# Optimization experiments

Hardware: AMD Instinct MI355X
Metric: run time of the kernel (lower is better)

Reference implementation:

```python
import jax, jax.numpy as jnp
import numpy as np

N = 150000   # total supergraph nodes (entities+events+chains)
D = 128      # embed_size
H = 4        # attention heads
DH = D // H  # head dim
E = 300000   # edges per layer
L = 4        # layer_specs length
A = 8        # edge attr dim
T = 10       # num_edge_type
TIME_SCALE = 24.0
SLOPE = 0.2  # negative_slope


def setup_inputs() -> dict:
    key = jax.random.key(0)
    ks = jax.random.split(key, 16)
    nrm = lambda k, s, sc=1.0: jax.random.normal(k, s, dtype=jnp.float32) * sc
    return {
        'x': nrm(ks[0], (N, D), 0.1),
        'Wq': nrm(ks[1], (L, D, D), D ** -0.5),
        'Wk': nrm(ks[2], (L, D, D), D ** -0.5),
        'Wv': nrm(ks[3], (L, D, D), D ** -0.5),
        'Wskip': nrm(ks[4], (L, D, D), D ** -0.5),
        'Wa': nrm(ks[5], (L, A, D), 0.1),
        'time_w': nrm(ks[6], (D,)),
        'time_b': nrm(ks[7], (D,), 0.1),
        'dist_w': nrm(ks[8], (D,)),
        'dist_b': nrm(ks[9], (D,), 0.1),
        'type_table': nrm(ks[10], (T, D), 0.1),
        'bn_gamma': jnp.ones((L, D), jnp.float32),
        'bn_beta': jnp.zeros((L, D), jnp.float32),
        'beta': jnp.full((L,), 0.5, jnp.float32),
        'edge_attr': jax.random.uniform(ks[11], (L, E, A), dtype=jnp.float32),
        'edge_dt': jax.random.uniform(ks[12], (L, E), dtype=jnp.float32) * TIME_SCALE,
        'edge_ds': jax.random.uniform(ks[13], (L, E), dtype=jnp.float32) * 10.0,
        'edge_index': jax.random.randint(ks[14], (L, 2, E), 0, N),
        'edge_type': jax.random.randint(ks[15], (L, E), 0, T),
    }


def _layer(x, Wq, Wk, Wv, Wskip, Wa, time_w, time_b, dist_w, dist_b,
           type_table, gamma, bvec, beta, attr, dt, ds, ei, et):
    n = x.shape[0]
    src, dst = ei[0], ei[1]
    # continuous time / distance encoders: cos basis (TimeEncoder / 'time' DistanceEncoder)
    te = jnp.cos((dt / TIME_SCALE)[:, None] * time_w + time_b)   # [E,D]
    de = jnp.cos(ds[:, None] * dist_w + dist_b)                  # [E,D]
    # 'add' edge/time fusion: attr MLP + time + dist + edge-type embeddings
    edge_feat = attr @ Wa + te + de + type_table[et]             # [E,D]
    kv_in = x[src] + edge_feat                                   # gather + fuse
    q = (x @ Wq).reshape(n, H, DH)[dst]                          # [E,H,DH]
    k = (kv_in @ Wk).reshape(-1, H, DH)
    v = (kv_in @ Wv).reshape(-1, H, DH)
    logits = (q * k).sum(-1) * (DH ** -0.5)                      # [E,H]
    logits = jnp.where(logits >= 0, logits, SLOPE * logits)      # leaky_relu(negative_slope)
    # segment softmax over incoming edges of each destination node
    m = jax.ops.segment_max(logits, dst, num_segments=n)
    a = jnp.exp(logits - m[dst])
    denom = jax.ops.segment_sum(a, dst, num_segments=n)
    a = a / denom[dst]
    agg = jax.ops.segment_sum(a[..., None] * v, dst, num_segments=n).reshape(n, D)
    # beta-weighted residual (learn_beta) with skip projection
    out = beta * (x @ Wskip) + (1.0 - beta) * agg
    # BatchNorm1d (training-mode batch stats) + ReLU
    mu = out.mean(0)
    var = out.var(0)
    out = (out - mu) * jax.lax.rsqrt(var + 1e-5) * gamma + bvec
    return jax.nn.relu(out)


def reference(x, Wq, Wk, Wv, Wskip, Wa, time_w, time_b, dist_w, dist_b,
              type_table, bn_gamma, bn_beta, beta, edge_attr, edge_dt,
              edge_ds, edge_index, edge_type):
    for l in range(L):  # entity2event, event2event, event2chain (time filter), chain2chain
        x = _layer(x, Wq[l], Wk[l], Wv[l], Wskip[l], Wa[l],
                   time_w, time_b, dist_w, dist_b, type_table,
                   bn_gamma[l], bn_beta[l], beta[l],
                   edge_attr[l], edge_dt[l], edge_ds[l],
                   edge_index[l], edge_type[l])
    return x
```

## Files before the change

kernel.cpp:

```cpp
#include <hip/hip_runtime.h>

typedef unsigned int u32;
typedef unsigned short u16;
typedef short bf16x8 __attribute__((ext_vector_type(8)));
typedef float f32x4 __attribute__((ext_vector_type(4)));

#define N_NODES 150000
#define E_EDGES 300000
#define L_CNT   151552

__device__ __forceinline__ float blo(u32 u){ return __uint_as_float(u << 16); }
__device__ __forceinline__ float bhi(u32 u){ return __uint_as_float(u & 0xffff0000u); }
__device__ __forceinline__ float b2f(u16 h){ return __uint_as_float(((u32)h) << 16); }
__device__ __forceinline__ u16 f2bf(float f){
  u32 u = __float_as_uint(f);
  return (u16)((u + 0x7fffu + ((u >> 16) & 1u)) >> 16);
}
__device__ __forceinline__ u32 pack2(float a, float b){
  return (u32)f2bf(a) | ((u32)f2bf(b) << 16);
}

__device__ __forceinline__ f32x4 mfma16(bf16x8 a, bf16x8 b, f32x4 c){
  return __builtin_amdgcn_mfma_f32_16x16x32_bf16(a, b, c, 0, 0, 0);
}

__device__ __forceinline__ int opsw(int r, int k){ return (r * 128 + k) ^ ((r & 7) << 3); }
__device__ __forceinline__ int csw(int r, int n){ return (r * 128 + n) ^ (((r >> 2) & 3) << 3); }

__global__ __launch_bounds__(256)
void k_wt(const float* __restrict__ Wq, const float* __restrict__ Wk,
          const float* __restrict__ Wv, const float* __restrict__ Ws,
          u16* __restrict__ Wt)
{
  const int m = blockIdx.x;
  const float* src = (m < 4 ? Wq : m < 8 ? Wk : m < 12 ? Wv : Ws)
                     + (size_t)(m & 3) * 16384;
  u16* dst = Wt + (size_t)m * 16384;
  const int t = threadIdx.x;
  for (int i = 0; i < 16; ++i) {
    int idx = i * 256 + t;
    int n = idx >> 5;
    int k4 = (idx & 31) << 2;
    ushort4 o;
    o.x = f2bf(src[(k4 + 0) * 128 + n]);
    o.y = f2bf(src[(k4 + 1) * 128 + n]);
    o.z = f2bf(src[(k4 + 2) * 128 + n]);
    o.w = f2bf(src[(k4 + 3) * 128 + n]);
    *(ushort4*)(dst + n * 128 + k4) = o;
  }
}

__device__ __forceinline__ void lds_to_global(const u16* Cs, u16* __restrict__ G,
                                              int base, int nr, int lane)
{
  #pragma unroll
  for (int i = 0; i < 8; ++i) {
    int idx = i * 64 + lane;
    int r = idx >> 4, n8 = (idx & 15) << 3;
    if (r < nr) {
      uint4 v = *(const uint4*)(Cs + csw(r, n8));
      *(uint4*)(G + (size_t)(base + r) * 128 + n8) = v;
    }
  }
}


__global__ __launch_bounds__(256)
void k_hist(const int* __restrict__ eidx, int* __restrict__ counts)
{
  const int l = blockIdx.y;
  const int e = blockIdx.x * 256 + threadIdx.x;
  if (e < E_EDGES) {
    int dst = eidx[(size_t)l * 2 * E_EDGES + E_EDGES + e];
    atomicAdd(&counts[(size_t)l * L_CNT + dst], 1);
  }
}

__global__ __launch_bounds__(256)
void k_scan1(const int* __restrict__ counts, int* __restrict__ rowptr,
             int* __restrict__ bsum)
{
  __shared__ int sh[256];
  const int b = blockIdx.x, l = blockIdx.y;
  const int t = threadIdx.x;
  const int* c = counts + (size_t)l * L_CNT + b * 2048;
  int* rp = rowptr + (size_t)l * L_CNT + b * 2048;
  int v[8]; int s = 0;
  #pragma unroll
  for (int j = 0; j < 8; ++j) { v[j] = c[t * 8 + j]; s += v[j]; }
  sh[t] = s; __syncthreads();
  for (int off = 1; off < 256; off <<= 1) {
    int x = (t >= off) ? sh[t - off] : 0;
    __syncthreads();
    sh[t] += x;
    __syncthreads();
  }
  int excl = (t == 0) ? 0 : sh[t - 1];
  if (t == 255) bsum[l * 128 + b] = sh[255];
  int run = excl;
  #pragma unroll
  for (int j = 0; j < 8; ++j) { rp[t * 8 + j] = run; run += v[j]; }
}

__global__ __launch_bounds__(128)
void k_scan2(int* __restrict__ bsum)
{
  __shared__ int sh[128];
  const int l = blockIdx.x, t = threadIdx.x;
  int v = (t < 74) ? bsum[l * 128 + t] : 0;
  sh[t] = v; __syncthreads();
  for (int off = 1; off < 128; off <<= 1) {
    int x = (t >= off) ? sh[t - off] : 0;
    __syncthreads();
    sh[t] += x;
    __syncthreads();
  }
  int excl = (t == 0) ? 0 : sh[t - 1];
  if (t < 74) bsum[l * 128 + t] = excl;
}

__global__ __launch_bounds__(256)
void k_scan3(int* __restrict__ rowptr, int* __restrict__ tmp,
             const int* __restrict__ bsum)
{
  const int l = blockIdx.y;
  const int q = blockIdx.x * 256 + threadIdx.x;
  int v = rowptr[(size_t)l * L_CNT + q] + bsum[l * 128 + (q >> 11)];
  rowptr[(size_t)l * L_CNT + q] = v;
  tmp[(size_t)l * L_CNT + q] = v;
}

__global__ __launch_bounds__(256)
void k_scatter(const int* __restrict__ srcP, const int* __restrict__ dstP,
               const int* __restrict__ etP, const float* __restrict__ dtP,
               const float* __restrict__ dsP, const float* __restrict__ attrP,
               int* __restrict__ tmpL, u32* __restrict__ meta)
{
  const int e = blockIdx.x * 256 + threadIdx.x;
  if (e < E_EDGES) {
    int dst = dstP[e];
    int pos = atomicAdd(&tmpL[dst], 1);
    int src = srcP[e];
    int et  = etP[e];
    float dtn = dtP[e] * (1.0f / 24.0f);
    float dsv = dsP[e];
    float4 aA = *(const float4*)(attrP + (size_t)e * 8);
    float4 aB = *(const float4*)(attrP + (size_t)e * 8 + 4);
    uint4 r0, r1;
    r0.x = (u32)src;
    r0.y = (u32)dst | ((u32)et << 20);
    r0.z = __float_as_uint(dtn);
    r0.w = __float_as_uint(dsv);
    r1.x = pack2(aA.x, aA.y); r1.y = pack2(aA.z, aA.w);
    r1.z = pack2(aB.x, aB.y); r1.w = pack2(aB.z, aB.w);
    u32* mp = meta + (size_t)pos * 8;
    *(uint4*)mp = r0;
    *(uint4*)(mp + 4) = r1;
  }
}


template<int XF32>
__global__ __launch_bounds__(128, 4)
void gemm_qs(const void* __restrict__ xg, const u16* __restrict__ WtQ,
             const u16* __restrict__ WtS, u16* __restrict__ Qo,
             u16* __restrict__ So)
{
  __shared__ __align__(16) u16 AsAll[2][4160];
  const u16* Wt = blockIdx.y ? WtS : WtQ;
  u16* C = blockIdx.y ? So : Qo;
  const int t = threadIdx.x;
  const int w = t >> 6, lane = t & 63;
  u16* As = AsAll[w];
  const int lr = lane & 15, hi = lane >> 4;
  const int tile = blockIdx.x * 2 + w;
  const int row0 = tile * 32;
  if (row0 >= N_NODES) return;
  const int nr = min(32, N_NODES - row0);
  const int g = lane >> 5;
  const int c4 = (lane & 31) << 2;

  #pragma unroll
  for (int i = 0; i < 16; ++i) {
    int r = i * 2 + g;
    ushort4 o = make_ushort4(0, 0, 0, 0);
    if (r < nr) {
      if (XF32) {
        float4 v = *(const float4*)((const float*)xg + (size_t)(row0 + r) * 128 + c4);
        o.x = f2bf(v.x); o.y = f2bf(v.y); o.z = f2bf(v.z); o.w = f2bf(v.w);
      } else {
        o = *(const ushort4*)((const u16*)xg + (size_t)(row0 + r) * 128 + c4);
      }
    }
    *(ushort4*)(As + opsw(r, c4)) = o;
  }

  f32x4 acc[2][8];
  #pragma unroll
  for (int a = 0; a < 2; ++a)
    #pragma unroll
    for (int b = 0; b < 8; ++b) {
      acc[a][b][0] = 0.f; acc[a][b][1] = 0.f;
      acc[a][b][2] = 0.f; acc[a][b][3] = 0.f;
    }
  #pragma unroll
  for (int ks = 0; ks < 4; ++ks) {
    const int kb = ks * 32 + hi * 8;
    bf16x8 a0 = *(const bf16x8*)(As + opsw(lr, kb));
    bf16x8 a1 = *(const bf16x8*)(As + opsw(16 + lr, kb));
    #pragma unroll
    for (int nb = 0; nb < 8; ++nb) {
      bf16x8 b = *(const bf16x8*)(Wt + (nb * 16 + lr) * 128 + kb);
      acc[0][nb] = mfma16(a0, b, acc[0][nb]);
      acc[1][nb] = mfma16(a1, b, acc[1][nb]);
    }
  }
  const int g4 = hi << 2;
  #pragma unroll
  for (int mt = 0; mt < 2; ++mt)
    #pragma unroll
    for (int nt = 0; nt < 8; ++nt)
      #pragma unroll
      for (int j = 0; j < 4; ++j)
        As[csw(mt * 16 + g4 + j, nt * 16 + lr)] = f2bf(acc[mt][nt][j]);
  lds_to_global(As, C, row0, nr, lane);
}


template<int XF32>
__global__ __launch_bounds__(128, 4)
void edge_pass(const void* __restrict__ xg, const u16* __restrict__ WtK,
               const u16* __restrict__ WtV, const float* __restrict__ Wa,
               const float* __restrict__ tw, const float* __restrict__ tb,
               const float* __restrict__ dw, const float* __restrict__ db,
               const float* __restrict__ ttab, const u32* __restrict__ meta,
               const u16* __restrict__ Qb, float* __restrict__ logits,
               u16* __restrict__ Vs)
{
  __shared__ __align__(16) u16 AsAll[2][4160];
  __shared__ int dstShAll[2][32];
  const int t = threadIdx.x;
  const int w = t >> 6, lane = t & 63;
  u16* As = AsAll[w];
  int* dstSh = dstShAll[w];
  const int lr = lane & 15, hi = lane >> 4;
  const int tile = blockIdx.x * 2 + w;
  const int e0 = tile * 32;
  if (e0 >= E_EDGES) return;
  const int ne = min(32, E_EDGES - e0);
  const int g = lane >> 5;
  const int c4 = (lane & 31) << 2;

  float4 tw4 = *(const float4*)(tw + c4);
  float4 tb4 = *(const float4*)(tb + c4);
  float4 dw4 = *(const float4*)(dw + c4);
  float4 db4 = *(const float4*)(db + c4);
  float4 wa4[8];
  #pragma unroll
  for (int a = 0; a < 8; ++a) wa4[a] = *(const float4*)(Wa + a * 128 + c4);

  #pragma unroll
  for (int i = 0; i < 16; ++i) {
    int r = i * 2 + g;
    ushort4 o = make_ushort4(0, 0, 0, 0);
    if (r < ne) {
      const u32* mp = meta + (size_t)(e0 + r) * 8;
      uint4 m0 = *(const uint4*)mp;
      uint4 m1 = *(const uint4*)(mp + 4);
      int src = (int)m0.x;
      if ((lane & 31) == 0) dstSh[r] = (int)(m0.y & 0xFFFFFu);
      int et = (int)(m0.y >> 20);
      float dtn = __uint_as_float(m0.z);
      float dss = __uint_as_float(m0.w);
      float4 tt4 = *(const float4*)(ttab + et * 128 + c4);
      float f0 = __cosf(fmaf(dtn, tw4.x, tb4.x)) + __cosf(fmaf(dss, dw4.x, db4.x)) + tt4.x;
      float f1 = __cosf(fmaf(dtn, tw4.y, tb4.y)) + __cosf(fmaf(dss, dw4.y, db4.y)) + tt4.y;
      float f2 = __cosf(fmaf(dtn, tw4.z, tb4.z)) + __cosf(fmaf(dss, dw4.z, db4.z)) + tt4.z;
      float f3 = __cosf(fmaf(dtn, tw4.w, tb4.w)) + __cosf(fmaf(dss, dw4.w, db4.w)) + tt4.w;
      float aa[8] = { blo(m1.x), bhi(m1.x), blo(m1.y), bhi(m1.y),
                      blo(m1.z), bhi(m1.z), blo(m1.w), bhi(m1.w) };
      #pragma unroll
      for (int a = 0; a < 8; ++a) {
        f0 = fmaf(aa[a], wa4[a].x, f0);
        f1 = fmaf(aa[a], wa4[a].y, f1);
        f2 = fmaf(aa[a], wa4[a].z, f2);
        f3 = fmaf(aa[a], wa4[a].w, f3);
      }
      float x0, x1, x2, x3;
      if (XF32) {
        float4 xr = *(const float4*)((const float*)xg + (size_t)src * 128 + c4);
        x0 = xr.x; x1 = xr.y; x2 = xr.z; x3 = xr.w;
      } else {
        ushort4 xr = *(const ushort4*)((const u16*)xg + (size_t)src * 128 + c4);
        x0 = b2f(xr.x); x1 = b2f(xr.y); x2 = b2f(xr.z); x3 = b2f(xr.w);
      }
      o.x = f2bf(x0 + f0);
      o.y = f2bf(x1 + f1);
      o.z = f2bf(x2 + f2);
      o.w = f2bf(x3 + f3);
    } else {
      if ((lane & 31) == 0) dstSh[r] = 0;
    }
    *(ushort4*)(As + opsw(r, c4)) = o;
  }

  #pragma unroll
  for (int eb = 0; eb < 2; ++eb) {
    f32x4 kacc[8];
    #pragma unroll
    for (int b = 0; b < 8; ++b) {
      kacc[b][0] = 0.f; kacc[b][1] = 0.f; kacc[b][2] = 0.f; kacc[b][3] = 0.f;
    }
    #pragma unroll
    for (int ks = 0; ks < 4; ++ks) {
      const int kb = ks * 32 + hi * 8;
      bf16x8 ef = *(const bf16x8*)(As + opsw(eb * 16 + lr, kb));
      #pragma unroll
      for (int nb = 0; nb < 8; ++nb) {
        bf16x8 af = *(const bf16x8*)(WtK + (nb * 16 + lr) * 128 + kb);
        kacc[nb] = mfma16(af, ef, kacc[nb]);
      }
    }
    int el = eb * 16 + lr;
    int dstn = dstSh[el];
    float hs[4] = {0.f, 0.f, 0.f, 0.f};
    #pragma unroll
    for (int nb = 0; nb < 8; ++nb) {
      ushort4 q = *(const ushort4*)(Qb + (size_t)dstn * 128 + nb * 16 + hi * 4);
      hs[nb >> 1] += b2f(q.x) * kacc[nb][0] + b2f(q.y) * kacc[nb][1]
                   + b2f(q.z) * kacc[nb][2] + b2f(q.w) * kacc[nb][3];
    }
    #pragma unroll
    for (int h = 0; h < 4; ++h) {
      hs[h] += __shfl_xor(hs[h], 16, 64);
      hs[h] += __shfl_xor(hs[h], 32, 64);
      hs[h] *= 0.17677669529663687f;
      hs[h] = (hs[h] >= 0.f) ? hs[h] : 0.2f * hs[h];
    }
    if (lane < 16 && el < ne)
      *(float4*)(logits + (size_t)(e0 + el) * 4) = make_float4(hs[0], hs[1], hs[2], hs[3]);
  }

  const int g4 = hi << 2;
  #pragma unroll
  for (int mt = 0; mt < 2; ++mt) {
    f32x4 vacc[8];
    #pragma unroll
    for (int b = 0; b < 8; ++b) {
      vacc[b][0] = 0.f; vacc[b][1] = 0.f; vacc[b][2] = 0.f; vacc[b][3] = 0.f;
    }
    #pragma unroll
    for (int ks = 0; ks < 4; ++ks) {
      const int kb = ks * 32 + hi * 8;
      bf16x8 af = *(const bf16x8*)(As + opsw(mt * 16 + lr, kb));
      #pragma unroll
      for (int nb = 0; nb < 8; ++nb) {
        bf16x8 bf = *(const bf16x8*)(WtV + (nb * 16 + lr) * 128 + kb);
        vacc[nb] = mfma16(af, bf, vacc[nb]);
      }
    }
    #pragma unroll
    for (int nt = 0; nt < 8; ++nt)
      #pragma unroll
      for (int j = 0; j < 4; ++j)
        As[csw(mt * 16 + g4 + j, nt * 16 + lr)] = f2bf(vacc[nt][j]);
  }
  lds_to_global(As, Vs, e0, ne, lane);
}

__global__ __launch_bounds__(256)
void node_agg(const u16* __restrict__ Vs, const float* __restrict__ logits,
              const int* __restrict__ rowptr, const u16* __restrict__ S,
              const float* __restrict__ betaP, float* __restrict__ pre,
              float* __restrict__ colsum, float* __restrict__ colsumsq)
{
  __shared__ float red[1024];
  const int t = threadIdx.x;
  const int g = t >> 5;
  const int lane = t & 31;
  const int d0 = lane * 4;
  const int h = lane >> 3;
  const float beta = *betaP;
  const float omb = 1.f - beta;
  float s4[4] = {0.f, 0.f, 0.f, 0.f};
  float q4[4] = {0.f, 0.f, 0.f, 0.f};
  for (int rep = 0; rep < 16; ++rep) {
    int n = blockIdx.x * 128 + rep * 8 + g;
    if (n < N_NODES) {
      int rs = rowptr[n], re = rowptr[n + 1];
      float m = -1e30f;
      for (int i = rs; i < re; ++i)
        m = fmaxf(m, logits[(size_t)i * 4 + h]);
      float den = 0.f;
      float a0 = 0.f, a1 = 0.f, a2 = 0.f, a3 = 0.f;
      for (int i = rs; i < re; ++i) {
        float wgt = __expf(logits[(size_t)i * 4 + h] - m);
        den += wgt;
        ushort4 v = *(const ushort4*)(Vs + (size_t)i * 128 + d0);
        a0 = fmaf(wgt, b2f(v.x), a0);
        a1 = fmaf(wgt, b2f(v.y), a1);
        a2 = fmaf(wgt, b2f(v.z), a2);
        a3 = fmaf(wgt, b2f(v.w), a3);
      }
      float inv = (den > 0.f) ? (omb / den) : 0.f;
      ushort4 sv = *(const ushort4*)(S + (size_t)n * 128 + d0);
      float p0 = fmaf(beta, b2f(sv.x), a0 * inv);
      float p1 = fmaf(beta, b2f(sv.y), a1 * inv);
      float p2 = fmaf(beta, b2f(sv.z), a2 * inv);
      float p3 = fmaf(beta, b2f(sv.w), a3 * inv);
      *(float4*)(pre + (size_t)n * 128 + d0) = make_float4(p0, p1, p2, p3);
      s4[0] += p0; s4[1] += p1; s4[2] += p2; s4[3] += p3;
      q4[0] += p0 * p0; q4[1] += p1 * p1; q4[2] += p2 * p2; q4[3] += p3 * p3;
    }
  }
  *(float4*)(&red[g * 128 + d0]) = make_float4(s4[0], s4[1], s4[2], s4[3]);
  __syncthreads();
  if (t < 128) {
    float tot = 0.f;
    #pragma unroll
    for (int gg = 0; gg < 8; ++gg) tot += red[gg * 128 + t];
    atomicAdd(&colsum[t], tot);
  }
  __syncthreads();
  *(float4*)(&red[g * 128 + d0]) = make_float4(q4[0], q4[1], q4[2], q4[3]);
  __syncthreads();
  if (t < 128) {
    float tot = 0.f;
    #pragma unroll
    for (int gg = 0; gg < 8; ++gg) tot += red[gg * 128 + t];
    atomicAdd(&colsumsq[t], tot);
  }
}

template<int LAST>
__global__ __launch_bounds__(256)
void bn_apply(const float* __restrict__ pre, const float* __restrict__ colsum,
              const float* __restrict__ colsumsq, const float* __restrict__ gamma,
              const float* __restrict__ bvec, u16* __restrict__ outbf,
              float* __restrict__ outf)
{
  const int idx = blockIdx.x * 256 + threadIdx.x;
  const int n = idx >> 5;
  const int d0 = (idx & 31) * 4;
  const float invN = 1.f / 150000.f;
  float4 p = *(const float4*)(pre + (size_t)n * 128 + d0);
  float4 cs = *(const float4*)(colsum + d0);
  float4 cq = *(const float4*)(colsumsq + d0);
  float4 gm = *(const float4*)(gamma + d0);
  float4 bv = *(const float4*)(bvec + d0);
  float mu, var, y;
  mu = cs.x * invN; var = cq.x * invN - mu * mu;
  y = (p.x - mu) * rsqrtf(var + 1e-5f) * gm.x + bv.x; p.x = fmaxf(y, 0.f);
  mu = cs.y * invN; var = cq.y * invN - mu * mu;
  y = (p.y - mu) * rsqrtf(var + 1e-5f) * gm.y + bv.y; p.y = fmaxf(y, 0.f);
  mu = cs.z * invN; var = cq.z * invN - mu * mu;
  y = (p.z - mu) * rsqrtf(var + 1e-5f) * gm.z + bv.z; p.z = fmaxf(y, 0.f);
  mu = cs.w * invN; var = cq.w * invN - mu * mu;
  y = (p.w - mu) * rsqrtf(var + 1e-5f) * gm.w + bv.w; p.w = fmaxf(y, 0.f);
  if (LAST) {
    *(float4*)(outf + (size_t)n * 128 + d0) = p;
  } else {
    ushort4 o;
    o.x = f2bf(p.x); o.y = f2bf(p.y); o.z = f2bf(p.z); o.w = f2bf(p.w);
    *(ushort4*)(outbf + (size_t)n * 128 + d0) = o;
  }
}

extern "C" void kernel_launch(void* const* d_in, const int* in_sizes, int n_in,
                              void* d_out, int out_size, void* d_ws, size_t ws_size,
                              hipStream_t stream)
{
  const float* x0    = (const float*)d_in[0];
  const float* Wq    = (const float*)d_in[1];
  const float* Wk    = (const float*)d_in[2];
  const float* Wv    = (const float*)d_in[3];
  const float* Wsk   = (const float*)d_in[4];
  const float* Wa    = (const float*)d_in[5];
  const float* tw    = (const float*)d_in[6];
  const float* tb    = (const float*)d_in[7];
  const float* dw    = (const float*)d_in[8];
  const float* db    = (const float*)d_in[9];
  const float* ttab  = (const float*)d_in[10];
  const float* gam   = (const float*)d_in[11];
  const float* bet   = (const float*)d_in[12];
  const float* betaP = (const float*)d_in[13];
  const float* attr  = (const float*)d_in[14];
  const float* dt    = (const float*)d_in[15];
  const float* dsv   = (const float*)d_in[16];
  const int*   eidx  = (const int*)d_in[17];
  const int*   etyp  = (const int*)d_in[18];

  char* p = (char*)d_ws;
  u16* xbf  = (u16*)p;       p += 38400000;
  u16* Q    = (u16*)p;       p += 38400000;
  u16* S    = (u16*)p;       p += 38400000;
  u16* Vs   = (u16*)p;       p += 76800000;
  float* logits = (float*)p; p += 4800000;
  int* rowptr = (int*)p;     p += 4 * L_CNT * 4;
  int* tmp    = (int*)p;     p += 4 * L_CNT * 4;
  int* bsum   = (int*)p;     p += 4 * 128 * 4;
  float* colsum   = (float*)p; p += 512;
  float* colsumsq = (float*)p; p += 512;
  u16* Wt = (u16*)p;         p += 16 * 16384 * 2;
  u32* meta = (u32*)p;       p += (size_t)E_EDGES * 32;

  float* pre = (float*)d_out;

  k_wt<<<16, 256, 0, stream>>>(Wq, Wk, Wv, Wsk, Wt);
  hipMemsetAsync(tmp, 0, 4 * L_CNT * 4, stream);
  k_hist<<<dim3(1172, 4), 256, 0, stream>>>(eidx, tmp);
  k_scan1<<<dim3(74, 4), 256, 0, stream>>>(tmp, rowptr, bsum);
  k_scan2<<<4, 128, 0, stream>>>(bsum);
  k_scan3<<<dim3(592, 4), 256, 0, stream>>>(rowptr, tmp, bsum);

  for (int l = 0; l < 4; ++l) {
    const int* srcA = eidx + (size_t)l * 600000;
    const int* dstA = srcA + 300000;
    const int* rpl = rowptr + (size_t)l * L_CNT;
    const u16* WtQl = Wt + (size_t)l * 16384;
    const u16* WtKl = Wt + (size_t)(4 + l) * 16384;
    const u16* WtVl = Wt + (size_t)(8 + l) * 16384;
    const u16* WtSl = Wt + (size_t)(12 + l) * 16384;
    const float* Wal = Wa + (size_t)l * 1024;

    k_scatter<<<1172, 256, 0, stream>>>(
        srcA, dstA, etyp + (size_t)l * 300000, dt + (size_t)l * 300000,
        dsv + (size_t)l * 300000, attr + (size_t)l * 2400000,
        tmp + (size_t)l * L_CNT, meta);

    hipMemsetAsync(colsum, 0, 1024, stream);

    if (l == 0) {
      gemm_qs<1><<<dim3(2344, 2), 128, 0, stream>>>((const void*)x0, WtQl, WtSl, Q, S);
      edge_pass<1><<<4688, 128, 0, stream>>>(
          (const void*)x0, WtKl, WtVl, Wal, tw, tb, dw, db, ttab, meta, Q, logits, Vs);
    } else {
      gemm_qs<0><<<dim3(2344, 2), 128, 0, stream>>>((const void*)xbf, WtQl, WtSl, Q, S);
      edge_pass<0><<<4688, 128, 0, stream>>>(
          (const void*)xbf, WtKl, WtVl, Wal, tw, tb, dw, db, ttab, meta, Q, logits, Vs);
    }

    node_agg<<<1172, 256, 0, stream>>>(Vs, logits, rpl, S, betaP + l,
                                       pre, colsum, colsumsq);

    if (l < 3)
      bn_apply<0><<<18750, 256, 0, stream>>>(pre, colsum, colsumsq,
                                             gam + (size_t)l * 128,
                                             bet + (size_t)l * 128, xbf, nullptr);
    else
      bn_apply<1><<<18750, 256, 0, stream>>>(pre, colsum, colsumsq,
                                             gam + (size_t)l * 128,
                                             bet + (size_t)l * 128,
                                             nullptr, (float*)d_out);
  }
}
```

Before: 1.701 ms.

## Split edge-feature construction into separate kernel before edge GEMM pass

Moves the per-edge kv_in construction (cos time/dist encodings, attr MLP, type embedding, source gather) out of edge_pass into a new fully parallel k_kvin kernel that writes bf16 kv_in to a global buffer. edge_pass then just loads the precomputed rows into LDS and does the K/V MFMAs, writing V back over the same buffer. The aim is to take the transcendental and gather-heavy prologue off the MFMA kernel, whose launch bounds limit occupancy, and run it at higher occupancy. In exchange it adds an extra global write and read of the E x 128 bf16 intermediate per layer, and it drops the tail bounds checks on the assumption that E is a multiple of 32 (300000 is not a multiple of 64, so the last edge_pass block depends on its existing early-return check).

```diff
diff --git a/kernel.cpp b/kernel.cpp
--- a/kernel.cpp
+++ b/kernel.cpp
@@ -51,16 +51,14 @@
 }
 
 __device__ __forceinline__ void lds_to_global(const u16* Cs, u16* __restrict__ G,
-                                              int base, int nr, int lane)
+                                              int base, int lane)
 {
   #pragma unroll
   for (int i = 0; i < 8; ++i) {
     int idx = i * 64 + lane;
     int r = idx >> 4, n8 = (idx & 15) << 3;
-    if (r < nr) {
-      uint4 v = *(const uint4*)(Cs + csw(r, n8));
-      *(uint4*)(G + (size_t)(base + r) * 128 + n8) = v;
-    }
+    uint4 v = *(const uint4*)(Cs + csw(r, n8));
+    *(uint4*)(G + (size_t)(base + r) * 128 + n8) = v;
   }
 }
 
@@ -159,6 +157,77 @@
   }
 }
 
+template<int XF32>
+__global__ __launch_bounds__(256)
+void k_kvin(const void* __restrict__ xg, const float* __restrict__ Wa,
+            const float* __restrict__ tw, const float* __restrict__ tb,
+            const float* __restrict__ dw, const float* __restrict__ db,
+            const float* __restrict__ ttab, const u32* __restrict__ meta,
+            u16* __restrict__ kvV)
+{
+  const int idx = blockIdx.x * 256 + threadIdx.x;
+  const int e = idx >> 4;
+  const int c8 = (idx & 15) << 3;
+  const u32* mp = meta + (size_t)e * 8;
+  uint4 m0 = *(const uint4*)mp;
+  uint4 m1 = *(const uint4*)(mp + 4);
+  const int src = (int)m0.x;
+  const int et = (int)(m0.y >> 20);
+  const float dtn = __uint_as_float(m0.z);
+  const float dss = __uint_as_float(m0.w);
+  float aa[8] = { blo(m1.x), bhi(m1.x), blo(m1.y), bhi(m1.y),
+                  blo(m1.z), bhi(m1.z), blo(m1.w), bhi(m1.w) };
+  const float4 twA = *(const float4*)(tw + c8);
+  const float4 twB = *(const float4*)(tw + c8 + 4);
+  const float4 tbA = *(const float4*)(tb + c8);
+  const float4 tbB = *(const float4*)(tb + c8 + 4);
+  const float4 dwA = *(const float4*)(dw + c8);
+  const float4 dwB = *(const float4*)(dw + c8 + 4);
+  const float4 dbA = *(const float4*)(db + c8);
+  const float4 dbB = *(const float4*)(db + c8 + 4);
+  const float4 ttA = *(const float4*)(ttab + et * 128 + c8);
+  const float4 ttB = *(const float4*)(ttab + et * 128 + c8 + 4);
+  float f[8];
+  f[0] = __cosf(fmaf(dtn, twA.x, tbA.x)) + __cosf(fmaf(dss, dwA.x, dbA.x)) + ttA.x;
+  f[1] = __cosf(fmaf(dtn, twA.y, tbA.y)) + __cosf(fmaf(dss, dwA.y, dbA.y)) + ttA.y;
+  f[2] = __cosf(fmaf(dtn, twA.z, tbA.z)) + __cosf(fmaf(dss, dwA.z, dbA.z)) + ttA.z;
+  f[3] = __cosf(fmaf(dtn, twA.w, tbA.w)) + __cosf(fmaf(dss, dwA.w, dbA.w)) + ttA.w;
+  f[4] = __cosf(fmaf(dtn, twB.x, tbB.x)) + __cosf(fmaf(dss, dwB.x, dbB.x)) + ttB.x;
+  f[5] = __cosf(fmaf(dtn, twB.y, tbB.y)) + __cosf(fmaf(dss, dwB.y, dbB.y)) + ttB.y;
+  f[6] = __cosf(fmaf(dtn, twB.z, tbB.z)) + __cosf(fmaf(dss, dwB.z, dbB.z)) + ttB.z;
+  f[7] = __cosf(fmaf(dtn, twB.w, tbB.w)) + __cosf(fmaf(dss, dwB.w, dbB.w)) + ttB.w;
+  #pragma unroll
+  for (int a = 0; a < 8; ++a) {
+    float4 wA = *(const float4*)(Wa + a * 128 + c8);
+    float4 wB = *(const float4*)(Wa + a * 128 + c8 + 4);
+    f[0] = fmaf(aa[a], wA.x, f[0]);
+    f[1] = fmaf(aa[a], wA.y, f[1]);
+    f[2] = fmaf(aa[a], wA.z, f[2]);
+    f[3] = fmaf(aa[a], wA.w, f[3]);
+    f[4] = fmaf(aa[a], wB.x, f[4]);
+    f[5] = fmaf(aa[a], wB.y, f[5]);
+    f[6] = fmaf(aa[a], wB.z, f[6]);
+    f[7] = fmaf(aa[a], wB.w, f[7]);
+  }
+  float xv[8];
+  if (XF32) {
+    float4 xA = *(const float4*)((const float*)xg + (size_t)src * 128 + c8);
+    float4 xB = *(const float4*)((const float*)xg + (size_t)src * 128 + c8 + 4);
+    xv[0] = xA.x; xv[1] = xA.y; xv[2] = xA.z; xv[3] = xA.w;
+    xv[4] = xB.x; xv[5] = xB.y; xv[6] = xB.z; xv[7] = xB.w;
+  } else {
+    uint4 xr = *(const uint4*)((const u16*)xg + (size_t)src * 128 + c8);
+    xv[0] = blo(xr.x); xv[1] = bhi(xr.x); xv[2] = blo(xr.y); xv[3] = bhi(xr.y);
+    xv[4] = blo(xr.z); xv[5] = bhi(xr.z); xv[6] = blo(xr.w); xv[7] = bhi(xr.w);
+  }
+  uint4 o;
+  o.x = pack2(xv[0] + f[0], xv[1] + f[1]);
+  o.y = pack2(xv[2] + f[2], xv[3] + f[3]);
+  o.z = pack2(xv[4] + f[4], xv[5] + f[5]);
+  o.w = pack2(xv[6] + f[6], xv[7] + f[7]);
+  *(uint4*)(kvV + (size_t)e * 128 + c8) = o;
+}
+
 
 template<int XF32>
 __global__ __launch_bounds__(128, 4)
@@ -223,19 +292,21 @@
       #pragma unroll
       for (int j = 0; j < 4; ++j)
         As[csw(mt * 16 + g4 + j, nt * 16 + lr)] = f2bf(acc[mt][nt][j]);
-  lds_to_global(As, C, row0, nr, lane);
-}
-
-
-template<int XF32>
+  #pragma unroll
+  for (int i = 0; i < 8; ++i) {
+    int idx = i * 64 + lane;
+    int r = idx >> 4, n8 = (idx & 15) << 3;
+    if (r < nr) {
+      uint4 v = *(const uint4*)(As + csw(r, n8));
+      *(uint4*)(C + (size_t)(row0 + r) * 128 + n8) = v;
+    }
+  }
+}
+
 __global__ __launch_bounds__(128, 4)
-void edge_pass(const void* __restrict__ xg, const u16* __restrict__ WtK,
-               const u16* __restrict__ WtV, const float* __restrict__ Wa,
-               const float* __restrict__ tw, const float* __restrict__ tb,
-               const float* __restrict__ dw, const float* __restrict__ db,
-               const float* __restrict__ ttab, const u32* __restrict__ meta,
-               const u16* __restrict__ Qb, float* __restrict__ logits,
-               u16* __restrict__ Vs)
+void edge_pass(const u16* __restrict__ WtK, const u16* __restrict__ WtV,
+               const u32* __restrict__ meta, const u16* __restrict__ Qb,
+               u16* __restrict__ kvV, float* __restrict__ logits)
 {
   __shared__ __align__(16) u16 AsAll[2][4160];
   __shared__ int dstShAll[2][32];
@@ -247,62 +318,16 @@
   const int tile = blockIdx.x * 2 + w;
   const int e0 = tile * 32;
   if (e0 >= E_EDGES) return;
-  const int ne = min(32, E_EDGES - e0);
-  const int g = lane >> 5;
-  const int c4 = (lane & 31) << 2;
-
-  float4 tw4 = *(const float4*)(tw + c4);
-  float4 tb4 = *(const float4*)(tb + c4);
-  float4 dw4 = *(const float4*)(dw + c4);
-  float4 db4 = *(const float4*)(db + c4);
-  float4 wa4[8];
-  #pragma unroll
-  for (int a = 0; a < 8; ++a) wa4[a] = *(const float4*)(Wa + a * 128 + c4);
-
-  #pragma unroll
-  for (int i = 0; i < 16; ++i) {
-    int r = i * 2 + g;
-    ushort4 o = make_ushort4(0, 0, 0, 0);
-    if (r < ne) {
-      const u32* mp = meta + (size_t)(e0 + r) * 8;
-      uint4 m0 = *(const uint4*)mp;
-      uint4 m1 = *(const uint4*)(mp + 4);
-      int src = (int)m0.x;
-      if ((lane & 31) == 0) dstSh[r] = (int)(m0.y & 0xFFFFFu);
-      int et = (int)(m0.y >> 20);
-      float dtn = __uint_as_float(m0.z);
-      float dss = __uint_as_float(m0.w);
-      float4 tt4 = *(const float4*)(ttab + et * 128 + c4);
-      float f0 = __cosf(fmaf(dtn, tw4.x, tb4.x)) + __cosf(fmaf(dss, dw4.x, db4.x)) + tt4.x;
-      float f1 = __cosf(fmaf(dtn, tw4.y, tb4.y)) + __cosf(fmaf(dss, dw4.y, db4.y)) + tt4.y;
-      float f2 = __cosf(fmaf(dtn, tw4.z, tb4.z)) + __cosf(fmaf(dss, dw4.z, db4.z)) + tt4.z;
-      float f3 = __cosf(fmaf(dtn, tw4.w, tb4.w)) + __cosf(fmaf(dss, dw4.w, db4.w)) + tt4.w;
-      float aa[8] = { blo(m1.x), bhi(m1.x), blo(m1.y), bhi(m1.y),
-                      blo(m1.z), bhi(m1.z), blo(m1.w), bhi(m1.w) };
-      #pragma unroll
-      for (int a = 0; a < 8; ++a) {
-        f0 = fmaf(aa[a], wa4[a].x, f0);
-        f1 = fmaf(aa[a], wa4[a].y, f1);
-        f2 = fmaf(aa[a], wa4[a].z, f2);
-        f3 = fmaf(aa[a], wa4[a].w, f3);
-      }
-      float x0, x1, x2, x3;
-      if (XF32) {
-        float4 xr = *(const float4*)((const float*)xg + (size_t)src * 128 + c4);
-        x0 = xr.x; x1 = xr.y; x2 = xr.z; x3 = xr.w;
-      } else {
-        ushort4 xr = *(const ushort4*)((const u16*)xg + (size_t)src * 128 + c4);
-        x0 = b2f(xr.x); x1 = b2f(xr.y); x2 = b2f(xr.z); x3 = b2f(xr.w);
-      }
-      o.x = f2bf(x0 + f0);
-      o.y = f2bf(x1 + f1);
-      o.z = f2bf(x2 + f2);
-      o.w = f2bf(x3 + f3);
-    } else {
-      if ((lane & 31) == 0) dstSh[r] = 0;
-    }
-    *(ushort4*)(As + opsw(r, c4)) = o;
-  }
+
+  #pragma unroll
+  for (int i = 0; i < 8; ++i) {
+    int idx = i * 64 + lane;
+    int r = idx >> 4, c8 = (idx & 15) << 3;
+    uint4 v = *(const uint4*)(kvV + (size_t)(e0 + r) * 128 + c8);
+    *(uint4*)(As + opsw(r, c8)) = v;
+  }
+  if (lane < 32)
+    dstSh[lane] = (int)(meta[(size_t)(e0 + lane) * 8 + 1] & 0xFFFFFu);
 
   #pragma unroll
   for (int eb = 0; eb < 2; ++eb) {
@@ -337,7 +362,7 @@
       hs[h] *= 0.17677669529663687f;
       hs[h] = (hs[h] >= 0.f) ? hs[h] : 0.2f * hs[h];
     }
-    if (lane < 16 && el < ne)
+    if (lane < 16)
       *(float4*)(logits + (size_t)(e0 + el) * 4) = make_float4(hs[0], hs[1], hs[2], hs[3]);
   }
 
@@ -365,7 +390,7 @@
       for (int j = 0; j < 4; ++j)
         As[csw(mt * 16 + g4 + j, nt * 16 + lr)] = f2bf(vacc[nt][j]);
   }
-  lds_to_global(As, Vs, e0, ne, lane);
+  lds_to_global(As, kvV, e0, lane);
 }
 
 __global__ __launch_bounds__(256)
@@ -494,7 +519,7 @@
   u16* xbf  = (u16*)p;       p += 38400000;
   u16* Q    = (u16*)p;       p += 38400000;
   u16* S    = (u16*)p;       p += 38400000;
-  u16* Vs   = (u16*)p;       p += 76800000;
+  u16* kvV  = (u16*)p;       p += 76800000;
   float* logits = (float*)p; p += 4800000;
   int* rowptr = (int*)p;     p += 4 * L_CNT * 4;
   int* tmp    = (int*)p;     p += 4 * L_CNT * 4;
@@ -531,16 +556,18 @@
     hipMemsetAsync(colsum, 0, 1024, stream);
 
     if (l == 0) {
+      k_kvin<1><<<18750, 256, 0, stream>>>((const void*)x0, Wal, tw, tb, dw, db,
+                                           ttab, meta, kvV);
       gemm_qs<1><<<dim3(2344, 2), 128, 0, stream>>>((const void*)x0, WtQl, WtSl, Q, S);
-      edge_pass<1><<<4688, 128, 0, stream>>>(
-          (const void*)x0, WtKl, WtVl, Wal, tw, tb, dw, db, ttab, meta, Q, logits, Vs);
     } else {
+      k_kvin<0><<<18750, 256, 0, stream>>>((const void*)xbf, Wal, tw, tb, dw, db,
+                                           ttab, meta, kvV);
       gemm_qs<0><<<dim3(2344, 2), 128, 0, stream>>>((const void*)xbf, WtQl, WtSl, Q, S);
-      edge_pass<0><<<4688, 128, 0, stream>>>(
-          (const void*)xbf, WtKl, WtVl, Wal, tw, tb, dw, db, ttab, meta, Q, logits, Vs);
-    }
-
-    node_agg<<<1172, 256, 0, stream>>>(Vs, logits, rpl, S, betaP + l,
+    }
+
+    edge_pass<<<4688, 128, 0, stream>>>(WtKl, WtVl, meta, Q, kvV, logits);
+
+    node_agg<<<1172, 256, 0, stream>>>(kvV, logits, rpl, S, betaP + l,
                                        pre, colsum, colsumsq);
 
     if (l < 3)
```

After: 1.976 ms. 1.16x slower.
